# Kernel tuning notes

Measured on AMD Instinct MI355X. Metric: run time of the kernel, lower is better.

## Reference

```python
import jax, jax.numpy as jnp
import numpy as np

B, S, D_IN, D, H, HD, HALF, L = 64, 500, 64, 128, 8, 16, 5, 2
WIN = 2 * HALF + 1  # 11 attended positions per query
EPS = 1e-12  # HF layer_norm_eps default


def _ln(x, g, b):
    m = x.mean(-1, keepdims=True)
    v = ((x - m) ** 2).mean(-1, keepdims=True)
    return (x - m) / jnp.sqrt(v + EPS) * g + b


def setup_inputs() -> dict:
    key = jax.random.key(0)
    ks = jax.random.split(key, 24)
    n = lambda i, shape: jax.random.normal(ks[i], shape, jnp.float32) * 0.02
    return {
        "x": jax.random.normal(ks[0], (B, S, D_IN), jnp.float32),
        "W_in": n(1, (D_IN, D)), "b_in": jnp.zeros((D,), jnp.float32),
        "pos_emb": n(2, (512, D)), "tt_emb": n(3, (D,)),
        "ln_emb_g": jnp.ones((D,), jnp.float32), "ln_emb_b": jnp.zeros((D,), jnp.float32),
        "Wq": n(4, (L, D, D)), "bq": jnp.zeros((L, D), jnp.float32),
        "Wk": n(5, (L, D, D)), "bk": jnp.zeros((L, D), jnp.float32),
        "Wv": n(6, (L, D, D)), "bv": jnp.zeros((L, D), jnp.float32),
        "Wo": n(7, (L, D, D)), "bo": jnp.zeros((L, D), jnp.float32),
        "ln1_g": jnp.ones((L, D), jnp.float32), "ln1_b": jnp.zeros((L, D), jnp.float32),
        "Wi": n(8, (L, D, 512)), "bi": jnp.zeros((L, 512), jnp.float32),
        "Wo2": n(9, (L, 512, D)), "bo2": jnp.zeros((L, D), jnp.float32),
        "ln2_g": jnp.ones((L, D), jnp.float32), "ln2_b": jnp.zeros((L, D), jnp.float32),
        "W_cls": n(10, (D, 2)), "b_cls": jnp.zeros((2,), jnp.float32),
    }


def reference(x, W_in, b_in, pos_emb, tt_emb, ln_emb_g, ln_emb_b,
              Wq, bq, Wk, bk, Wv, bv, Wo, bo, ln1_g, ln1_b,
              Wi, bi, Wo2, bo2, ln2_g, ln2_b, W_cls, b_cls):
    # input projection + RoBERTa-style embeddings (position ids start at padding_idx+1=2)
    h = x @ W_in + b_in
    pos_ids = 2 + jnp.arange(S)
    h = _ln(h + pos_emb[pos_ids] + tt_emb, ln_emb_g, ln_emb_b)

    # sliding-window gather indices: each query attends [i-HALF, i+HALF]
    idx = jnp.arange(S)[:, None] + jnp.arange(-HALF, HALF + 1)[None, :]
    valid = (idx >= 0) & (idx < S)
    idxc = jnp.clip(idx, 0, S - 1)
    scale = 1.0 / jnp.sqrt(jnp.float32(HD))

    for l in range(L):
        qh = (h @ Wq[l] + bq[l]).reshape(B, S, H, HD).transpose(0, 2, 1, 3)
        kh = (h @ Wk[l] + bk[l]).reshape(B, S, H, HD).transpose(0, 2, 1, 3)
        vh = (h @ Wv[l] + bv[l]).reshape(B, S, H, HD).transpose(0, 2, 1, 3)
        kk = kh[:, :, idxc]
        scores = jnp.einsum('bhsd,bhswd->bhsw', qh * scale, kk)
        scores = jnp.where(valid, scores, -jnp.inf)
        probs = jax.nn.softmax(scores, axis=-1)
        vv = vh[:, :, idxc]
        ctx = jnp.einsum('bhsw,bhswd->bhsd', probs, vv)
        ctx = ctx.transpose(0, 2, 1, 3).reshape(B, S, D)
        h = _ln(ctx @ Wo[l] + bo[l] + h, ln1_g[l], ln1_b[l])
        ff = jax.nn.gelu(h @ Wi[l] + bi[l], approximate=False) @ Wo2[l] + bo2[l]
        h = _ln(ff + h, ln2_g[l], ln2_b[l])

    pooled = h.mean(axis=1)  # mean over sequence
    return pooled @ W_cls + b_cls
```

## Files before the change

kernel.cpp:

```cpp
#include <hip/hip_runtime.h>
#include <hip/hip_bf16.h>
#include <math.h>

#define BB 64
#define SS 500
#define DIN 64
#define DD 128
#define HH 8
#define HDIM 16
#define HALF_ 5
#define WINW 11
#define LL 2
#define FF 512
#define MM (BB*SS)
#define LN_EPS 1e-12f

typedef __attribute__((ext_vector_type(8))) short short8;
typedef __attribute__((ext_vector_type(4))) float f32x4;

__global__ __launch_bounds__(256) void k_prep(
    const float* __restrict__ Wq, const float* __restrict__ Wk,
    const float* __restrict__ Wv, const float* __restrict__ Wo,
    const float* __restrict__ Wi, const float* __restrict__ Wo2,
    const float* __restrict__ Win, __hip_bfloat16* __restrict__ wT)
{
    const int m = blockIdx.y;
    const float* src; int Kd, Nd, kshift, doff;
    if (m == 12) {
        src = Win; Kd = 64; Nd = 128; kshift = 6; doff = 393216;
    } else {
        const int l = m / 6, t = m % 6;
        int toff;
        switch (t) {
          case 0:  src = Wq  + l*16384; Kd=128; Nd=128; kshift=7; toff=0;      break;
          case 1:  src = Wk  + l*16384; Kd=128; Nd=128; kshift=7; toff=16384;  break;
          case 2:  src = Wv  + l*16384; Kd=128; Nd=128; kshift=7; toff=32768;  break;
          case 3:  src = Wo  + l*16384; Kd=128; Nd=128; kshift=7; toff=49152;  break;
          case 4:  src = Wi  + l*65536; Kd=128; Nd=512; kshift=7; toff=65536;  break;
          default: src = Wo2 + l*65536; Kd=512; Nd=128; kshift=9; toff=131072; break;
        }
        doff = l*196608 + toff;
    }
    __hip_bfloat16* dst = wT + doff;
    const int NK = Kd * Nd;
    int e = (blockIdx.x * 256 + threadIdx.x) * 4;
    if (e >= NK) return;
    #pragma unroll
    for (int j = 0; j < 4; ++j, ++e) {
        int n = e >> kshift, kx = e & (Kd - 1);
        dst[(size_t)n * Kd + kx] = __float2bfloat16(src[(size_t)kx * Nd + n]);
    }
}

__global__ __launch_bounds__(256) void k_xcvt(
    const float* __restrict__ x, __hip_bfloat16* __restrict__ xbf)
{
    int i = (blockIdx.x * 256 + threadIdx.x) * 4;
    if (i >= MM * DIN) return;
    float4 v = *(const float4*)(x + i);
    ushort4 o;
    __hip_bfloat16 t0 = __float2bfloat16(v.x); o.x = *(unsigned short*)&t0;
    __hip_bfloat16 t1 = __float2bfloat16(v.y); o.y = *(unsigned short*)&t1;
    __hip_bfloat16 t2 = __float2bfloat16(v.z); o.z = *(unsigned short*)&t2;
    __hip_bfloat16 t3 = __float2bfloat16(v.w); o.w = *(unsigned short*)&t3;
    *(ushort4*)(xbf + i) = o;
}

#define GEMM_MAIN(Abf, lda, Kdim, WTbf, ldw, n0w)                             \
    __shared__ __align__(16) __hip_bfloat16 As[64][72];                       \
    __shared__ __align__(16) __hip_bfloat16 Ws[128][72];                      \
    const int tid = threadIdx.x;                                              \
    const int wid = tid >> 6;                                                 \
    const int l15 = tid & 15;                                                 \
    const int l4  = (tid & 63) >> 4;                                          \
    const int m0  = blockIdx.x * 64;                                          \
    f32x4 acc[8];                                                             \
    _Pragma("unroll")                                                         \
    for (int n = 0; n < 8; ++n) acc[n] = (f32x4){0.f, 0.f, 0.f, 0.f};         \
    for (int k0 = 0; k0 < (Kdim); k0 += 64) {                                 \
        _Pragma("unroll")                                                     \
        for (int it = 0; it < 2; ++it) {                                      \
            int lin = it * 2048 + tid * 8;                                    \
            int r = lin >> 6, c = lin & 63;                                   \
            *(uint4*)&As[r][c] =                                              \
                *(const uint4*)((Abf) + (size_t)(m0 + r) * (lda) + k0 + c);   \
        }                                                                     \
        _Pragma("unroll")                                                     \
        for (int it = 0; it < 4; ++it) {                                      \
            int lin = it * 2048 + tid * 8;                                    \
            int r = lin >> 6, c = lin & 63;                                   \
            *(uint4*)&Ws[r][c] =                                              \
                *(const uint4*)((WTbf) + (size_t)((n0w) + r) * (ldw) + k0 + c); \
        }                                                                     \
        __syncthreads();                                                      \
        _Pragma("unroll")                                                     \
        for (int kc = 0; kc < 64; kc += 32) {                                 \
            short8 a0 = *(const short8*)&As[wid * 16 + l15][kc + l4 * 8];     \
            _Pragma("unroll")                                                 \
            for (int n = 0; n < 8; ++n) {                                     \
                short8 bf = *(const short8*)&Ws[n * 16 + l15][kc + l4 * 8];   \
                acc[n] = __builtin_amdgcn_mfma_f32_16x16x32_bf16(a0, bf, acc[n], 0, 0, 0); \
            }                                                                 \
        }                                                                     \
        __syncthreads();                                                      \
    }

__global__ __launch_bounds__(256, 4) void k_embed(
    const __hip_bfloat16* __restrict__ xbf, const __hip_bfloat16* __restrict__ wInT,
    const float* __restrict__ bin, const float* __restrict__ pos,
    const float* __restrict__ tt, const float* __restrict__ g,
    const float* __restrict__ be, float* __restrict__ h,
    __hip_bfloat16* __restrict__ hbf)
{
    GEMM_MAIN(xbf, DIN, DIN, wInT, DIN, 0)
    #pragma unroll
    for (int qq = 0; qq < 4; ++qq) {
        const int row = m0 + wid * 16 + l4 * 4 + qq;
        const int s = row % SS;
        float vals[8]; float s1 = 0.f, s2 = 0.f;
        #pragma unroll
        for (int n = 0; n < 8; ++n) {
            const int col = n * 16 + l15;
            float val = acc[n][qq] + bin[col] + tt[col] + pos[(size_t)(2 + s) * DD + col];
            vals[n] = val; s1 += val; s2 += val * val;
        }
        #pragma unroll
        for (int o = 1; o < 16; o <<= 1) {
            s1 += __shfl_xor(s1, o, 16);
            s2 += __shfl_xor(s2, o, 16);
        }
        const float mean = s1 * (1.0f / DD);
        const float var  = s2 * (1.0f / DD) - mean * mean;
        const float rstd = rsqrtf(var + LN_EPS);
        #pragma unroll
        for (int n = 0; n < 8; ++n) {
            const int col = n * 16 + l15;
            const float o = (vals[n] - mean) * rstd * g[col] + be[col];
            h[(size_t)row * DD + col]   = o;
            hbf[(size_t)row * DD + col] = __float2bfloat16(o);
        }
    }
}

__global__ __launch_bounds__(512, 4) void k_fused(
    const __hip_bfloat16* __restrict__ hin,
    const __hip_bfloat16* __restrict__ wTq, const __hip_bfloat16* __restrict__ wTk,
    const __hip_bfloat16* __restrict__ wTv, const __hip_bfloat16* __restrict__ wTo,
    const __hip_bfloat16* __restrict__ wTi, const __hip_bfloat16* __restrict__ wTo2,
    const float* __restrict__ bq, const float* __restrict__ bk,
    const float* __restrict__ bv, const float* __restrict__ bo,
    const float* __restrict__ bi, const float* __restrict__ bo2,
    const float* __restrict__ hres,
    const float* __restrict__ g1, const float* __restrict__ bt1,
    const float* __restrict__ g2, const float* __restrict__ bt2,
    float* __restrict__ hout, __hip_bfloat16* __restrict__ hbfout)
{
    __shared__ __align__(16) char smem[51072];
    __hip_bfloat16* kS   = (__hip_bfloat16*)smem;
    __hip_bfloat16* vS   = (__hip_bfloat16*)(smem + 13056);
    __hip_bfloat16* hS   = (__hip_bfloat16*)(smem + 26112);
    __hip_bfloat16* qS   = (__hip_bfloat16*)(smem + 39168);
    float*          pS   = (float*)(smem + 47872);
    float*          rsum = (float*)(smem + 50048);
    __hip_bfloat16* ctxS = hS;
    __hip_bfloat16* h1S  = qS;
    __hip_bfloat16* hidS = (__hip_bfloat16*)smem;

    const int tid = threadIdx.x;
    const int wid = tid >> 6;
    const int l15 = tid & 15, l4 = (tid & 63) >> 4;
    const int b = blockIdx.y;
    const int s0 = blockIdx.x * 32;

    #pragma unroll
    for (int it = 0; it < 2; ++it) {
        int lin = it * 512 + tid;
        if (lin < 768) {
            int r = lin >> 4, c8 = (lin & 15) * 8;
            int s = s0 - 5 + r;
            uint4 val = {0, 0, 0, 0};
            if (s >= 0 && s < SS)
                val = *(const uint4*)(hin + ((size_t)(b * SS + s)) * DD + c8);
            *(uint4*)&hS[r * 136 + c8] = val;
        }
    }
    __syncthreads();

    #pragma unroll
    for (int i = 0; i < 9; ++i) {
        const int t = wid + i * 8;
        const int out = t / 24;
        const int rem = t - out * 24;
        const int rt = rem >> 3, n = rem & 7;
        const __hip_bfloat16* WT = (out == 0) ? wTq : ((out == 1) ? wTk : wTv);
        const float* bias = (out == 0) ? bq : ((out == 1) ? bk : bv);
        f32x4 a = (f32x4){0.f, 0.f, 0.f, 0.f};
        #pragma unroll
        for (int kc = 0; kc < 4; ++kc) {
            short8 af  = *(const short8*)&hS[(rt * 16 + l15) * 136 + kc * 32 + l4 * 8];
            short8 bfg = *(const short8*)(WT + (size_t)(n * 16 + l15) * DD + kc * 32 + l4 * 8);
            a = __builtin_amdgcn_mfma_f32_16x16x32_bf16(af, bfg, a, 0, 0, 0);
        }
        const int col = n * 16 + l15;
        const float bcol = bias[col];
        #pragma unroll
        for (int qq = 0; qq < 4; ++qq) {
            const int row = rt * 16 + l4 * 4 + qq;
            const float val = a[qq] + bcol;
            if (out == 0) {
                if (row >= 5 && row < 37)
                    qS[(row - 5) * 136 + col] = __float2bfloat16(val * 0.25f);
            } else if (out == 1) {
                kS[row * 136 + col] = __float2bfloat16(val);
            } else {
                vS[row * 136 + col] = __float2bfloat16(val);
            }
        }
    }
    __syncthreads();

    {
        const int g = tid >> 4, wl = tid & 15;
        const int sq = s0 + g;
        const int sk = sq + wl - HALF_;
        const bool valid = (wl < WINW) && (sq < SS) && (sk >= 0) && (sk < SS);
        #pragma unroll
        for (int hh = 0; hh < 8; ++hh) {
            const int off = hh * 16;
            float sc = 0.f;
            const unsigned* qp = (const unsigned*)&qS[g * 136 + off];
            const unsigned* kp = (const unsigned*)&kS[(g + wl) * 136 + off];
            #pragma unroll
            for (int d2 = 0; d2 < 8; ++d2) {
                unsigned qu = qp[d2], ku = kp[d2];
                sc += __uint_as_float(qu << 16) * __uint_as_float(ku << 16)
                    + __uint_as_float(qu & 0xffff0000u) * __uint_as_float(ku & 0xffff0000u);
            }
            sc = valid ? sc : -INFINITY;
            float mx = sc;
            #pragma unroll
            for (int o = 1; o < 16; o <<= 1) mx = fmaxf(mx, __shfl_xor(mx, o, 16));
            float p = valid ? __expf(sc - mx) : 0.f;
            float den = p;
            #pragma unroll
            for (int o = 1; o < 16; o <<= 1) den += __shfl_xor(den, o, 16);
            const float inv = (den > 0.f) ? 1.f / den : 0.f;
            pS[g * 17 + wl] = p;
            float cd = 0.f;
            #pragma unroll
            for (int w2 = 0; w2 < WINW; ++w2)
                cd += pS[g * 17 + w2] * __bfloat162float(vS[(g + w2) * 136 + off + wl]);
            ctxS[g * 136 + off + wl] = __float2bfloat16(cd * inv);
        }
    }
    __syncthreads();

    const int rt2 = wid & 1, nh = wid >> 1;
    {
        f32x4 ac[2];
        #pragma unroll
        for (int n4 = 0; n4 < 2; ++n4) {
            ac[n4] = (f32x4){0.f, 0.f, 0.f, 0.f};
            const int n = nh * 2 + n4;
            #pragma unroll
            for (int kc = 0; kc < 4; ++kc) {
                short8 af  = *(const short8*)&ctxS[(rt2 * 16 + l15) * 136 + kc * 32 + l4 * 8];
                short8 bfg = *(const short8*)(wTo + (size_t)(n * 16 + l15) * DD + kc * 32 + l4 * 8);
                ac[n4] = __builtin_amdgcn_mfma_f32_16x16x32_bf16(af, bfg, ac[n4], 0, 0, 0);
            }
        }
        float vals[4][2];
        #pragma unroll
        for (int qq = 0; qq < 4; ++qq) {
            const int r16 = l4 * 4 + qq;
            const int qrow = rt2 * 16 + r16;
            const int sq = s0 + qrow;
            const bool vr = (sq < SS);
            float s1 = 0.f, s2 = 0.f;
            #pragma unroll
            for (int n4 = 0; n4 < 2; ++n4) {
                const int col = (nh * 2 + n4) * 16 + l15;
                const float resv = vr ? hres[((size_t)(b * SS + sq)) * DD + col] : 0.f;
                const float val = ac[n4][qq] + bo[col] + resv;
                vals[qq][n4] = val; s1 += val; s2 += val * val;
            }
            #pragma unroll
            for (int o = 1; o < 16; o <<= 1) {
                s1 += __shfl_xor(s1, o, 16);
                s2 += __shfl_xor(s2, o, 16);
            }
            if (l15 == 0) {
                rsum[((rt2 * 4 + nh) * 16 + r16) * 2]     = s1;
                rsum[((rt2 * 4 + nh) * 16 + r16) * 2 + 1] = s2;
            }
        }
        __syncthreads();
        #pragma unroll
        for (int qq = 0; qq < 4; ++qq) {
            const int r16 = l4 * 4 + qq;
            const int qrow = rt2 * 16 + r16;
            float S1 = 0.f, S2 = 0.f;
            #pragma unroll
            for (int j = 0; j < 4; ++j) {
                S1 += rsum[((rt2 * 4 + j) * 16 + r16) * 2];
                S2 += rsum[((rt2 * 4 + j) * 16 + r16) * 2 + 1];
            }
            const float mean = S1 * (1.0f / DD);
            const float var  = S2 * (1.0f / DD) - mean * mean;
            const float rstd = rsqrtf(fmaxf(var, 0.f) + LN_EPS);
            #pragma unroll
            for (int n4 = 0; n4 < 2; ++n4) {
                const int col = (nh * 2 + n4) * 16 + l15;
                const float o = (vals[qq][n4] - mean) * rstd * g1[col] + bt1[col];
                vals[qq][n4] = o;
                h1S[qrow * 136 + col] = __float2bfloat16(o);
            }
        }
        __syncthreads();

        #pragma unroll
        for (int i = 0; i < 8; ++i) {
            const int t = wid + i * 8;
            const int rt = t >> 5, n = t & 31;
            f32x4 a = (f32x4){0.f, 0.f, 0.f, 0.f};
            #pragma unroll
            for (int kc = 0; kc < 4; ++kc) {
                short8 af  = *(const short8*)&h1S[(rt * 16 + l15) * 136 + kc * 32 + l4 * 8];
                short8 bfg = *(const short8*)(wTi + (size_t)(n * 16 + l15) * DD + kc * 32 + l4 * 8);
                a = __builtin_amdgcn_mfma_f32_16x16x32_bf16(af, bfg, a, 0, 0, 0);
            }
            const int col = n * 16 + l15;
            const float bcol = bi[col];
            #pragma unroll
            for (int qq = 0; qq < 4; ++qq) {
                const int row = rt * 16 + l4 * 4 + qq;
                float val = a[qq] + bcol;
                val = 0.5f * val * (1.f + erff(val * 0.70710678118f));
                hidS[row * 520 + col] = __float2bfloat16(val);
            }
        }
        __syncthreads();

        f32x4 a2[2];
        #pragma unroll
        for (int n4 = 0; n4 < 2; ++n4) {
            a2[n4] = (f32x4){0.f, 0.f, 0.f, 0.f};
            const int n = nh * 2 + n4;
            #pragma unroll
            for (int ks = 0; ks < 16; ++ks) {
                short8 af  = *(const short8*)&hidS[(rt2 * 16 + l15) * 520 + ks * 32 + l4 * 8];
                short8 bfg = *(const short8*)(wTo2 + (size_t)(n * 16 + l15) * FF + ks * 32 + l4 * 8);
                a2[n4] = __builtin_amdgcn_mfma_f32_16x16x32_bf16(af, bfg, a2[n4], 0, 0, 0);
            }
        }
        float vals2[4][2];
        __syncthreads();
        #pragma unroll
        for (int qq = 0; qq < 4; ++qq) {
            const int r16 = l4 * 4 + qq;
            float s1 = 0.f, s2 = 0.f;
            #pragma unroll
            for (int n4 = 0; n4 < 2; ++n4) {
                const int col = (nh * 2 + n4) * 16 + l15;
                const float val = a2[n4][qq] + bo2[col] + vals[qq][n4];
                vals2[qq][n4] = val; s1 += val; s2 += val * val;
            }
            #pragma unroll
            for (int o = 1; o < 16; o <<= 1) {
                s1 += __shfl_xor(s1, o, 16);
                s2 += __shfl_xor(s2, o, 16);
            }
            if (l15 == 0) {
                rsum[((rt2 * 4 + nh) * 16 + r16) * 2]     = s1;
                rsum[((rt2 * 4 + nh) * 16 + r16) * 2 + 1] = s2;
            }
        }
        __syncthreads();
        #pragma unroll
        for (int qq = 0; qq < 4; ++qq) {
            const int r16 = l4 * 4 + qq;
            const int qrow = rt2 * 16 + r16;
            const int sq = s0 + qrow;
            if (sq >= SS) continue;
            float S1 = 0.f, S2 = 0.f;
            #pragma unroll
            for (int j = 0; j < 4; ++j) {
                S1 += rsum[((rt2 * 4 + j) * 16 + r16) * 2];
                S2 += rsum[((rt2 * 4 + j) * 16 + r16) * 2 + 1];
            }
            const float mean = S1 * (1.0f / DD);
            const float var  = S2 * (1.0f / DD) - mean * mean;
            const float rstd = rsqrtf(fmaxf(var, 0.f) + LN_EPS);
            #pragma unroll
            for (int n4 = 0; n4 < 2; ++n4) {
                const int col = (nh * 2 + n4) * 16 + l15;
                const float o = (vals2[qq][n4] - mean) * rstd * g2[col] + bt2[col];
                hout[((size_t)(b * SS + sq)) * DD + col]   = o;
                hbfout[((size_t)(b * SS + sq)) * DD + col] = __float2bfloat16(o);
            }
        }
    }
}

__global__ __launch_bounds__(128) void k_final(
    const float* __restrict__ h, const float* __restrict__ Wc,
    const float* __restrict__ bc, float* __restrict__ out)
{
    const int b = blockIdx.x, d = threadIdx.x;
    float p = 0.f;
    for (int s = 0; s < SS; ++s) p += h[((size_t)(b * SS + s)) * DD + d];
    p *= (1.0f / SS);
    float l0 = p * Wc[d * 2 + 0];
    float l1 = p * Wc[d * 2 + 1];
    #pragma unroll
    for (int off = 1; off < 64; off <<= 1) {
        l0 += __shfl_xor(l0, off);
        l1 += __shfl_xor(l1, off);
    }
    __shared__ float r[2][2];
    const int wid = d >> 6;
    if ((d & 63) == 0) { r[wid][0] = l0; r[wid][1] = l1; }
    __syncthreads();
    if (d == 0) {
        out[b * 2 + 0] = r[0][0] + r[1][0] + bc[0];
        out[b * 2 + 1] = r[0][1] + r[1][1] + bc[1];
    }
}

extern "C" void kernel_launch(void* const* d_in, const int* in_sizes, int n_in,
                              void* d_out, int out_size, void* d_ws, size_t ws_size,
                              hipStream_t stream)
{
    const float* x      = (const float*)d_in[0];
    const float* W_in   = (const float*)d_in[1];
    const float* b_in   = (const float*)d_in[2];
    const float* pos    = (const float*)d_in[3];
    const float* tt     = (const float*)d_in[4];
    const float* lng    = (const float*)d_in[5];
    const float* lnb    = (const float*)d_in[6];
    const float* Wq     = (const float*)d_in[7];
    const float* bq     = (const float*)d_in[8];
    const float* Wk     = (const float*)d_in[9];
    const float* bk     = (const float*)d_in[10];
    const float* Wv     = (const float*)d_in[11];
    const float* bv     = (const float*)d_in[12];
    const float* Wo     = (const float*)d_in[13];
    const float* bo     = (const float*)d_in[14];
    const float* ln1g   = (const float*)d_in[15];
    const float* ln1b   = (const float*)d_in[16];
    const float* Wi     = (const float*)d_in[17];
    const float* bi     = (const float*)d_in[18];
    const float* Wo2    = (const float*)d_in[19];
    const float* bo2    = (const float*)d_in[20];
    const float* ln2g   = (const float*)d_in[21];
    const float* ln2b   = (const float*)d_in[22];
    const float* Wc     = (const float*)d_in[23];
    const float* bc     = (const float*)d_in[24];

    float*          ws   = (float*)d_ws;
    float*          hA   = ws;
    __hip_bfloat16* hbA  = (__hip_bfloat16*)(ws + 4096000);
    __hip_bfloat16* xbf  = (__hip_bfloat16*)(ws + 6144000);
    __hip_bfloat16* wT   = (__hip_bfloat16*)(ws + 7168000);
    float*          hB   = ws + 7368704;
    __hip_bfloat16* hbB  = (__hip_bfloat16*)(ws + 11464704);

    k_prep<<<dim3(64, 13), 256, 0, stream>>>(Wq, Wk, Wv, Wo, Wi, Wo2, W_in, wT);
    k_xcvt<<<2000, 256, 0, stream>>>(x, xbf);
    k_embed<<<MM / 64, 256, 0, stream>>>(xbf, wT + 393216, b_in, pos, tt, lng, lnb,
                                         hA, hbA);

    float* hI = hA; __hip_bfloat16* hbI = hbA;
    float* hO = hB; __hip_bfloat16* hbO = hbB;
    for (int l = 0; l < LL; ++l) {
        const __hip_bfloat16* wTq  = wT + l * 196608;
        const __hip_bfloat16* wTk  = wTq + 16384;
        const __hip_bfloat16* wTv  = wTq + 32768;
        const __hip_bfloat16* wTo  = wTq + 49152;
        const __hip_bfloat16* wTi  = wTq + 65536;
        const __hip_bfloat16* wTo2 = wTq + 131072;

        k_fused<<<dim3(16, BB), 512, 0, stream>>>(
            hbI, wTq, wTk, wTv, wTo, wTi, wTo2,
            bq + l * DD, bk + l * DD, bv + l * DD, bo + l * DD,
            bi + l * FF, bo2 + l * DD,
            hI, ln1g + l * DD, ln1b + l * DD, ln2g + l * DD, ln2b + l * DD,
            hO, hbO);

        float* tf = hI; hI = hO; hO = tf;
        __hip_bfloat16* tb = hbI; hbI = hbO; hbO = tb;
    }

    k_final<<<BB, 128, 0, stream>>>(hI, Wc, bc, (float*)d_out);
}
```

Before: 346.2 us.

## Shrink fused-layer LDS footprint to raise occupancy and split FFN into halves

The fused layer kernel no longer stages the input rows in shared memory; the QKV projection reads its A operands straight from global memory and zeroes rows outside the sequence. Attention probabilities are passed between lanes with shuffles instead of an LDS scratch, and the context is kept in registers until K/V buffers can be reused. The FFN hidden activation is computed in two 256-column halves, with the second GEMM accumulating across halves, so LDS drops from about 51KB to about 39KB and launch bounds ask for 8 waves per EU. The cost is redundant global reads of the h rows, extra barriers, and possible register pressure or spills under the tighter bound.

```diff
diff --git a/kernel.cpp b/kernel.cpp
--- a/kernel.cpp
+++ b/kernel.cpp
@@ -142,7 +142,7 @@
     }
 }
 
-__global__ __launch_bounds__(512, 4) void k_fused(
+__global__ __launch_bounds__(512, 8) void k_fused(
     const __hip_bfloat16* __restrict__ hin,
     const __hip_bfloat16* __restrict__ wTq, const __hip_bfloat16* __restrict__ wTk,
     const __hip_bfloat16* __restrict__ wTv, const __hip_bfloat16* __restrict__ wTo,
@@ -155,36 +155,21 @@
     const float* __restrict__ g2, const float* __restrict__ bt2,
     float* __restrict__ hout, __hip_bfloat16* __restrict__ hbfout)
 {
-    __shared__ __align__(16) char smem[51072];
+    __shared__ __align__(16) char smem[39680];
     __hip_bfloat16* kS   = (__hip_bfloat16*)smem;
     __hip_bfloat16* vS   = (__hip_bfloat16*)(smem + 13056);
-    __hip_bfloat16* hS   = (__hip_bfloat16*)(smem + 26112);
-    __hip_bfloat16* qS   = (__hip_bfloat16*)(smem + 39168);
-    float*          pS   = (float*)(smem + 47872);
-    float*          rsum = (float*)(smem + 50048);
-    __hip_bfloat16* ctxS = hS;
-    __hip_bfloat16* h1S  = qS;
-    __hip_bfloat16* hidS = (__hip_bfloat16*)smem;
+    __hip_bfloat16* qS   = (__hip_bfloat16*)(smem + 26112);
+    __hip_bfloat16* hidS = (__hip_bfloat16*)(smem + 21760);
+    float*          rsum = (float*)(smem + 38656);
+    __hip_bfloat16* ctxS = kS;
+    __hip_bfloat16* h1S  = vS;
 
     const int tid = threadIdx.x;
     const int wid = tid >> 6;
     const int l15 = tid & 15, l4 = (tid & 63) >> 4;
     const int b = blockIdx.y;
     const int s0 = blockIdx.x * 32;
-
-    #pragma unroll
-    for (int it = 0; it < 2; ++it) {
-        int lin = it * 512 + tid;
-        if (lin < 768) {
-            int r = lin >> 4, c8 = (lin & 15) * 8;
-            int s = s0 - 5 + r;
-            uint4 val = {0, 0, 0, 0};
-            if (s >= 0 && s < SS)
-                val = *(const uint4*)(hin + ((size_t)(b * SS + s)) * DD + c8);
-            *(uint4*)&hS[r * 136 + c8] = val;
-        }
-    }
-    __syncthreads();
+    const short8 zero8 = {0,0,0,0,0,0,0,0};
 
     #pragma unroll
     for (int i = 0; i < 9; ++i) {
@@ -194,10 +179,14 @@
         const int rt = rem >> 3, n = rem & 7;
         const __hip_bfloat16* WT = (out == 0) ? wTq : ((out == 1) ? wTk : wTv);
         const float* bias = (out == 0) ? bq : ((out == 1) ? bk : bv);
+        const int srow = s0 - 5 + rt * 16 + l15;
+        const bool rok = (srow >= 0) && (srow < SS);
+        const __hip_bfloat16* arow = hin + ((size_t)(b * SS) + (rok ? srow : 0)) * DD;
         f32x4 a = (f32x4){0.f, 0.f, 0.f, 0.f};
         #pragma unroll
         for (int kc = 0; kc < 4; ++kc) {
-            short8 af  = *(const short8*)&hS[(rt * 16 + l15) * 136 + kc * 32 + l4 * 8];
+            short8 af = *(const short8*)(arow + kc * 32 + l4 * 8);
+            if (!rok) af = zero8;
             short8 bfg = *(const short8*)(WT + (size_t)(n * 16 + l15) * DD + kc * 32 + l4 * 8);
             a = __builtin_amdgcn_mfma_f32_16x16x32_bf16(af, bfg, a, 0, 0, 0);
         }
@@ -219,6 +208,7 @@
     }
     __syncthreads();
 
+    float ctxv[8];
     {
         const int g = tid >> 4, wl = tid & 15;
         const int sq = s0 + g;
@@ -227,15 +217,17 @@
         #pragma unroll
         for (int hh = 0; hh < 8; ++hh) {
             const int off = hh * 16;
+            const uint4* qp = (const uint4*)&qS[g * 136 + off];
+            const uint4* kp = (const uint4*)&kS[(g + wl) * 136 + off];
+            uint4 qv0 = qp[0], qv1 = qp[1];
+            uint4 kv0 = kp[0], kv1 = kp[1];
             float sc = 0.f;
-            const unsigned* qp = (const unsigned*)&qS[g * 136 + off];
-            const unsigned* kp = (const unsigned*)&kS[(g + wl) * 136 + off];
-            #pragma unroll
-            for (int d2 = 0; d2 < 8; ++d2) {
-                unsigned qu = qp[d2], ku = kp[d2];
-                sc += __uint_as_float(qu << 16) * __uint_as_float(ku << 16)
-                    + __uint_as_float(qu & 0xffff0000u) * __uint_as_float(ku & 0xffff0000u);
-            }
+            #define DOTD(qu, ku)                                              \
+                sc += __uint_as_float((qu) << 16) * __uint_as_float((ku) << 16) \
+                    + __uint_as_float((qu) & 0xffff0000u) * __uint_as_float((ku) & 0xffff0000u);
+            DOTD(qv0.x, kv0.x) DOTD(qv0.y, kv0.y) DOTD(qv0.z, kv0.z) DOTD(qv0.w, kv0.w)
+            DOTD(qv1.x, kv1.x) DOTD(qv1.y, kv1.y) DOTD(qv1.z, kv1.z) DOTD(qv1.w, kv1.w)
+            #undef DOTD
             sc = valid ? sc : -INFINITY;
             float mx = sc;
             #pragma unroll
@@ -245,17 +237,25 @@
             #pragma unroll
             for (int o = 1; o < 16; o <<= 1) den += __shfl_xor(den, o, 16);
             const float inv = (den > 0.f) ? 1.f / den : 0.f;
-            pS[g * 17 + wl] = p;
             float cd = 0.f;
             #pragma unroll
             for (int w2 = 0; w2 < WINW; ++w2)
-                cd += pS[g * 17 + w2] * __bfloat162float(vS[(g + w2) * 136 + off + wl]);
-            ctxS[g * 136 + off + wl] = __float2bfloat16(cd * inv);
-        }
+                cd += __shfl(p, w2, 16) * __bfloat162float(vS[(g + w2) * 136 + off + wl]);
+            ctxv[hh] = cd * inv;
+        }
+    }
+    __syncthreads();
+
+    {
+        const int g = tid >> 4, wl = tid & 15;
+        #pragma unroll
+        for (int hh = 0; hh < 8; ++hh)
+            ctxS[g * 136 + hh * 16 + wl] = __float2bfloat16(ctxv[hh]);
     }
     __syncthreads();
 
     const int rt2 = wid & 1, nh = wid >> 1;
+    float vals[4][2];
     {
         f32x4 ac[2];
         #pragma unroll
@@ -269,7 +269,6 @@
                 ac[n4] = __builtin_amdgcn_mfma_f32_16x16x32_bf16(af, bfg, ac[n4], 0, 0, 0);
             }
         }
-        float vals[4][2];
         #pragma unroll
         for (int qq = 0; qq < 4; ++qq) {
             const int r16 = l4 * 4 + qq;
@@ -294,34 +293,42 @@
                 rsum[((rt2 * 4 + nh) * 16 + r16) * 2 + 1] = s2;
             }
         }
-        __syncthreads();
-        #pragma unroll
-        for (int qq = 0; qq < 4; ++qq) {
-            const int r16 = l4 * 4 + qq;
-            const int qrow = rt2 * 16 + r16;
-            float S1 = 0.f, S2 = 0.f;
-            #pragma unroll
-            for (int j = 0; j < 4; ++j) {
-                S1 += rsum[((rt2 * 4 + j) * 16 + r16) * 2];
-                S2 += rsum[((rt2 * 4 + j) * 16 + r16) * 2 + 1];
-            }
-            const float mean = S1 * (1.0f / DD);
-            const float var  = S2 * (1.0f / DD) - mean * mean;
-            const float rstd = rsqrtf(fmaxf(var, 0.f) + LN_EPS);
-            #pragma unroll
-            for (int n4 = 0; n4 < 2; ++n4) {
-                const int col = (nh * 2 + n4) * 16 + l15;
-                const float o = (vals[qq][n4] - mean) * rstd * g1[col] + bt1[col];
-                vals[qq][n4] = o;
-                h1S[qrow * 136 + col] = __float2bfloat16(o);
-            }
-        }
-        __syncthreads();
-
-        #pragma unroll
-        for (int i = 0; i < 8; ++i) {
+    }
+    __syncthreads();
+    #pragma unroll
+    for (int qq = 0; qq < 4; ++qq) {
+        const int r16 = l4 * 4 + qq;
+        const int qrow = rt2 * 16 + r16;
+        float S1 = 0.f, S2 = 0.f;
+        #pragma unroll
+        for (int j = 0; j < 4; ++j) {
+            S1 += rsum[((rt2 * 4 + j) * 16 + r16) * 2];
+            S2 += rsum[((rt2 * 4 + j) * 16 + r16) * 2 + 1];
+        }
+        const float mean = S1 * (1.0f / DD);
+        const float var  = S2 * (1.0f / DD) - mean * mean;
+        const float rstd = rsqrtf(fmaxf(var, 0.f) + LN_EPS);
+        #pragma unroll
+        for (int n4 = 0; n4 < 2; ++n4) {
+            const int col = (nh * 2 + n4) * 16 + l15;
+            const float o = (vals[qq][n4] - mean) * rstd * g1[col] + bt1[col];
+            vals[qq][n4] = o;
+            h1S[qrow * 136 + col] = __float2bfloat16(o);
+        }
+    }
+    __syncthreads();
+
+    f32x4 a2[2];
+    #pragma unroll
+    for (int n4 = 0; n4 < 2; ++n4) a2[n4] = (f32x4){0.f, 0.f, 0.f, 0.f};
+
+    #pragma unroll
+    for (int half = 0; half < 2; ++half) {
+        #pragma unroll
+        for (int i = 0; i < 4; ++i) {
             const int t = wid + i * 8;
-            const int rt = t >> 5, n = t & 31;
+            const int rt = t >> 4, nloc = t & 15;
+            const int n = half * 16 + nloc;
             f32x4 a = (f32x4){0.f, 0.f, 0.f, 0.f};
             #pragma unroll
             for (int kc = 0; kc < 4; ++kc) {
@@ -329,75 +336,75 @@
                 short8 bfg = *(const short8*)(wTi + (size_t)(n * 16 + l15) * DD + kc * 32 + l4 * 8);
                 a = __builtin_amdgcn_mfma_f32_16x16x32_bf16(af, bfg, a, 0, 0, 0);
             }
-            const int col = n * 16 + l15;
-            const float bcol = bi[col];
+            const int colg = n * 16 + l15;
+            const int lc   = nloc * 16 + l15;
+            const float bcol = bi[colg];
             #pragma unroll
             for (int qq = 0; qq < 4; ++qq) {
                 const int row = rt * 16 + l4 * 4 + qq;
                 float val = a[qq] + bcol;
                 val = 0.5f * val * (1.f + erff(val * 0.70710678118f));
-                hidS[row * 520 + col] = __float2bfloat16(val);
+                hidS[row * 264 + lc] = __float2bfloat16(val);
             }
         }
         __syncthreads();
-
-        f32x4 a2[2];
         #pragma unroll
         for (int n4 = 0; n4 < 2; ++n4) {
-            a2[n4] = (f32x4){0.f, 0.f, 0.f, 0.f};
             const int n = nh * 2 + n4;
             #pragma unroll
-            for (int ks = 0; ks < 16; ++ks) {
-                short8 af  = *(const short8*)&hidS[(rt2 * 16 + l15) * 520 + ks * 32 + l4 * 8];
-                short8 bfg = *(const short8*)(wTo2 + (size_t)(n * 16 + l15) * FF + ks * 32 + l4 * 8);
+            for (int ksl = 0; ksl < 8; ++ksl) {
+                short8 af  = *(const short8*)&hidS[(rt2 * 16 + l15) * 264 + ksl * 32 + l4 * 8];
+                short8 bfg = *(const short8*)(wTo2 + (size_t)(n * 16 + l15) * FF
+                                              + half * 256 + ksl * 32 + l4 * 8);
                 a2[n4] = __builtin_amdgcn_mfma_f32_16x16x32_bf16(af, bfg, a2[n4], 0, 0, 0);
             }
         }
-        float vals2[4][2];
         __syncthreads();
-        #pragma unroll
-        for (int qq = 0; qq < 4; ++qq) {
-            const int r16 = l4 * 4 + qq;
-            float s1 = 0.f, s2 = 0.f;
-            #pragma unroll
-            for (int n4 = 0; n4 < 2; ++n4) {
-                const int col = (nh * 2 + n4) * 16 + l15;
-                const float val = a2[n4][qq] + bo2[col] + vals[qq][n4];
-                vals2[qq][n4] = val; s1 += val; s2 += val * val;
-            }
-            #pragma unroll
-            for (int o = 1; o < 16; o <<= 1) {
-                s1 += __shfl_xor(s1, o, 16);
-                s2 += __shfl_xor(s2, o, 16);
-            }
-            if (l15 == 0) {
-                rsum[((rt2 * 4 + nh) * 16 + r16) * 2]     = s1;
-                rsum[((rt2 * 4 + nh) * 16 + r16) * 2 + 1] = s2;
-            }
-        }
-        __syncthreads();
-        #pragma unroll
-        for (int qq = 0; qq < 4; ++qq) {
-            const int r16 = l4 * 4 + qq;
-            const int qrow = rt2 * 16 + r16;
-            const int sq = s0 + qrow;
-            if (sq >= SS) continue;
-            float S1 = 0.f, S2 = 0.f;
-            #pragma unroll
-            for (int j = 0; j < 4; ++j) {
-                S1 += rsum[((rt2 * 4 + j) * 16 + r16) * 2];
-                S2 += rsum[((rt2 * 4 + j) * 16 + r16) * 2 + 1];
-            }
-            const float mean = S1 * (1.0f / DD);
-            const float var  = S2 * (1.0f / DD) - mean * mean;
-            const float rstd = rsqrtf(fmaxf(var, 0.f) + LN_EPS);
-            #pragma unroll
-            for (int n4 = 0; n4 < 2; ++n4) {
-                const int col = (nh * 2 + n4) * 16 + l15;
-                const float o = (vals2[qq][n4] - mean) * rstd * g2[col] + bt2[col];
-                hout[((size_t)(b * SS + sq)) * DD + col]   = o;
-                hbfout[((size_t)(b * SS + sq)) * DD + col] = __float2bfloat16(o);
-            }
+    }
+
+    float vals2[4][2];
+    #pragma unroll
+    for (int qq = 0; qq < 4; ++qq) {
+        const int r16 = l4 * 4 + qq;
+        float s1 = 0.f, s2 = 0.f;
+        #pragma unroll
+        for (int n4 = 0; n4 < 2; ++n4) {
+            const int col = (nh * 2 + n4) * 16 + l15;
+            const float val = a2[n4][qq] + bo2[col] + vals[qq][n4];
+            vals2[qq][n4] = val; s1 += val; s2 += val * val;
+        }
+        #pragma unroll
+        for (int o = 1; o < 16; o <<= 1) {
+            s1 += __shfl_xor(s1, o, 16);
+            s2 += __shfl_xor(s2, o, 16);
+        }
+        if (l15 == 0) {
+            rsum[((rt2 * 4 + nh) * 16 + r16) * 2]     = s1;
+            rsum[((rt2 * 4 + nh) * 16 + r16) * 2 + 1] = s2;
+        }
+    }
+    __syncthreads();
+    #pragma unroll
+    for (int qq = 0; qq < 4; ++qq) {
+        const int r16 = l4 * 4 + qq;
+        const int qrow = rt2 * 16 + r16;
+        const int sq = s0 + qrow;
+        if (sq >= SS) continue;
+        float S1 = 0.f, S2 = 0.f;
+        #pragma unroll
+        for (int j = 0; j < 4; ++j) {
+            S1 += rsum[((rt2 * 4 + j) * 16 + r16) * 2];
+            S2 += rsum[((rt2 * 4 + j) * 16 + r16) * 2 + 1];
+        }
+        const float mean = S1 * (1.0f / DD);
+        const float var  = S2 * (1.0f / DD) - mean * mean;
+        const float rstd = rsqrtf(fmaxf(var, 0.f) + LN_EPS);
+        #pragma unroll
+        for (int n4 = 0; n4 < 2; ++n4) {
+            const int col = (nh * 2 + n4) * 16 + l15;
+            const float o = (vals2[qq][n4] - mean) * rstd * g2[col] + bt2[col];
+            hout[((size_t)(b * SS + sq)) * DD + col]   = o;
+            hbfout[((size_t)(b * SS + sq)) * DD + col] = __float2bfloat16(o);
         }
     }
 }
```

Measured after the change: 417.6 us. 20.6% more time.
